# Kernel tuning notes

Measured on AMD Instinct MI355X. Metric: run time of the kernel, lower is better.

The kernel has to match this reference:

```python
import jax, jax.numpy as jnp
import numpy as np

ALPHA = 0.25
GAMMA = 2.0
LAMBDA_T = 0.1


def count_components(fg):
    """Count 6-connected components per volume. fg: [M,H,W,D] bool.
    Min-label propagation + pointer jumping (parallel union-find style CCL),
    matching scipy.ndimage.label's default face-connectivity structure.
    Returns float32 [M] component counts."""
    M, H, W, D = fg.shape
    N = H * W * D
    BIG = jnp.int32(N)  # sentinel label for background / padding
    idx = jnp.arange(N, dtype=jnp.int32).reshape(1, H, W, D)
    L0 = jnp.broadcast_to(idx, fg.shape)

    def shift(a, axis, d):
        # b[i] = a[i-d] along `axis`, padded with BIG outside the volume
        pad = [(0, 0)] * 4
        pad[axis] = (max(d, 0), max(-d, 0))
        ap = jnp.pad(a, pad, constant_values=N)
        sl = [slice(None)] * 4
        sl[axis] = slice(max(-d, 0), max(-d, 0) + a.shape[axis])
        return ap[tuple(sl)]

    def one_step(L):
        Lv = jnp.where(fg, L, BIG)
        m = Lv
        for ax in (1, 2, 3):
            for d in (1, -1):
                m = jnp.minimum(m, shift(Lv, ax, d))
        Ln = jnpp_min = jnp.where(fg, jnp.minimum(L, m), L)
        # pointer jumping (L <- L[L]) twice for log-depth convergence
        Lf = Ln.reshape(M, N)
        Lf = jnp.take_along_axis(Lf, Lf, axis=1)
        Lf = jnp.take_along_axis(Lf, Lf, axis=1)
        return Lf.reshape(M, H, W, D)

    def cond(s):
        return s[1]

    def body(s):
        L, _ = s
        Ln = one_step(L)
        return (Ln, jnp.any(Ln != L))

    L, _ = jax.lax.while_loop(cond, body, (L0, jnp.bool_(True)))
    # at fixed point every foreground component carries its min linear index;
    # roots satisfy L[i] == i
    roots = fg & (L == idx)
    return jnp.sum(roots, axis=(1, 2, 3)).astype(jnp.float32)


def _focal(x, t):
    p = jax.nn.sigmoid(x)
    pt = jnp.where(t == 1, p, 1.0 - p)
    bce = jax.nn.softplus(x) - x * t  # BCE-with-logits, elementwise
    alpha_t = jnp.where(t == 1, ALPHA, 1.0 - ALPHA)
    return jnp.mean(alpha_t * (1.0 - pt) ** GAMMA * bce)


def _topology(x, t):
    B, C = x.shape[:2]
    spatial = x.shape[2:]
    fg_p = (jax.nn.sigmoid(x) > 0.5).reshape(B * C, *spatial)
    fg_t = (t > 0.5).reshape(B * C, *spatial)
    cc_p = count_components(fg_p).reshape(B, C).mean(axis=0)  # mean over batch per class
    cc_t = count_components(fg_t).reshape(B, C).mean(axis=0)
    return jnp.mean(jnp.abs(cc_p - cc_t))  # sum over classes / C


def setup_inputs() -> dict:
    key = jax.random.key(0)
    k1, k2 = jax.random.split(key)
    shape = (2, 2, 96, 96, 96)
    pred_logits = jax.random.normal(k1, shape, dtype=jnp.float32)
    target_binary = jax.random.randint(k2, shape, 0, 2).astype(jnp.float32)
    return {"pred_logits": pred_logits, "target_binary": target_binary}


def reference(pred_logits, target_binary):
    focal = _focal(pred_logits, target_binary)
    topo = jax.lax.stop_gradient(_topology(pred_logits, target_binary))
    return focal + LAMBDA_T * topo
```

## Files before the change

### kernel.cpp

```cpp
#include <hip/hip_runtime.h>
#include <math.h>

#define N_VOX (96*96*96)
#define NVOL 8
#define NEL (4*N_VOX)
#define PLANE (96*96)
#define GMWORDS (N_VOX/32)
#define NFACC (4*GMWORDS/256)

#define TW 8
#define TH 8
#define TILES_W 12
#define TILES_H 12
#define TILE_VOX (96*TW*TH)
#define TILE_WORDS (TILE_VOX/32)
#define MAXRUNS 3072

#define NBPLANES 11
#define NPAIRS (2*NBPLANES)
#define FACES_PER_VOL (2*NPAIRS*PLANE)
#define MAXR 40192
#define FALLR 65536
#define SEGCAP 4608
#define HT2N 4096
#define MAX_PROBES 16

#define WS_ROOT  1024
#define WS_COMP  2048
#define WS_DONE  3072
#define WS_VDONE 4096
#define WS_PCNT  4352
#define WS_FACC  5120
#define WS_HDR   8192

__device__ __forceinline__ int uf_find(int* __restrict__ L, int x) {
    int r = x;
    int p = L[r];
    while (p != r) { r = p; p = L[r]; }
    if (r != x) atomicMin(&L[x], r);
    return r;
}

__device__ __forceinline__ int uf_merge(int* __restrict__ L, int l1, int l2) {
    int ev = 0;
    while (l1 != l2) {
        if (l1 < l2) { int t = l1; l1 = l2; l2 = t; }
        int l3 = atomicMin(&L[l1], l2);
        if (l3 == l1) { ev++; l1 = l2; }
        else l1 = l3;
    }
    return ev;
}

__device__ __forceinline__ void merge_local(int* lab, int l1, int l2) {
    while (l1 != l2 && l1 != lab[l1]) l1 = lab[l1];
    while (l1 != l2 && l2 != lab[l2]) l2 = lab[l2];
    while (l1 != l2) {
        if (l1 < l2) { int t = l1; l1 = l2; l2 = t; }
        int l3 = atomicMin(&lab[l1], l2);
        l1 = (l3 == l1) ? l2 : l3;
    }
}

__device__ __forceinline__ int rrank(const unsigned* __restrict__ sm,
                                     const int* __restrict__ wpf, int i) {
    int w = i >> 5, b = i & 31;
    unsigned mask = (2u << b) - 1u;
    return wpf[w] + __popc(sm[w] & mask) - 1;
}

__global__ __launch_bounds__(256) void fgmask_focal(const float* __restrict__ pred,
                                                    const float* __restrict__ targ,
                                                    unsigned* __restrict__ gmask,
                                                    float* __restrict__ facc,
                                                    int* __restrict__ rootcnt,
                                                    int* __restrict__ done,
                                                    int* __restrict__ vdone) {
    __shared__ float fws[4];
    if (blockIdx.x == 0 && threadIdx.x == 0) {
        for (int v2 = 0; v2 < NVOL; v2++) { rootcnt[v2 << 5] = 0; done[v2 << 5] = 0; }
        *vdone = 0;
    }
    int tid = blockIdx.x * 256 + threadIdx.x;
    int v = tid / GMWORDS;
    int w = tid - v * GMWORDS;
    const float4* P = (const float4*)(pred + (size_t)v * N_VOX + w * 32);
    const float4* T = (const float4*)(targ + (size_t)v * N_VOX + w * 32);
    unsigned pb = 0, tb = 0;
    float fsum = 0.0f;
    #pragma unroll
    for (int j4 = 0; j4 < 8; j4++) {
        float4 p4 = P[j4];
        float4 t4 = T[j4];
        float pv[4] = {p4.x, p4.y, p4.z, p4.w};
        float tv[4] = {t4.x, t4.y, t4.z, t4.w};
        #pragma unroll
        for (int q = 0; q < 4; q++) {
            int j = j4 * 4 + q;
            if (pv[q] > 0.0f)  pb |= (1u << j);
            if (tv[q] > 0.5f)  tb |= (1u << j);
            float m   = (tv[q] == 1.0f) ? -pv[q] : pv[q];
            float at  = (tv[q] == 1.0f) ? 0.25f : 0.75f;
            float e   = __expf(-fabsf(m));
            float inv = 1.0f / (1.0f + e);
            float sig = inv * ((m >= 0.0f) ? 1.0f : e);
            float sp  = fmaxf(m, 0.0f) + __logf(1.0f + e);
            fsum += at * sig * sig * sp;
        }
    }
    gmask[(size_t)v * GMWORDS + w]       = pb;
    gmask[(size_t)(v + 4) * GMWORDS + w] = tb;

    for (int off = 32; off; off >>= 1) fsum += __shfl_down(fsum, off, 64);
    if ((threadIdx.x & 63) == 0) fws[threadIdx.x >> 6] = fsum;
    __syncthreads();
    if (threadIdx.x == 0)
        facc[blockIdx.x] = fws[0] + fws[1] + fws[2] + fws[3];
}

__global__ __launch_bounds__(256) void ccl_local(const unsigned* __restrict__ gmask,
                                                 unsigned short* __restrict__ faces,
                                                 int* __restrict__ rootcnt,
                                                 int vbase) {
    __shared__ int      lab[MAXRUNS];
    __shared__ unsigned fm[TILE_WORDS];
    __shared__ unsigned sm[TILE_WORDS];
    __shared__ int      wpf[TILE_WORDS];
    __shared__ unsigned ovst[168];
    __shared__ int      ovpf[169];
    __shared__ int   iws[4];
    __shared__ int   gbase;

    int vloc = blockIdx.y;
    int v = vbase + vloc;
    int tile = blockIdx.x;
    int tw = tile % TILES_W, th = tile / TILES_W;
    int w0 = tw * TW, h0 = th * TH;
    int tbase = h0 * PLANE + w0 * 96;
    unsigned short* Fw = faces + (size_t)vloc * FACES_PER_VOL;
    unsigned short* Fh = Fw + 2 * NBPLANES * PLANE;
    const unsigned* gm = gmask + (size_t)v * GMWORDS;

    if (threadIdx.x < TILE_WORDS) {
        int t = threadIdx.x;
        int lh = t / 24, rem = t % 24;
        fm[t] = gm[(tbase >> 5) + lh * 288 + rem];
    }
    for (int r = threadIdx.x; r < MAXRUNS; r += 256) lab[r] = r;
    __syncthreads();

    int cnt = 0;
    {
        unsigned st = 0;
        if (threadIdx.x < TILE_WORDS) {
            unsigned m = fm[threadIdx.x];
            unsigned carry = (threadIdx.x % 3) ? (fm[threadIdx.x - 1] >> 31) : 0u;
            st = m & ~((m << 1) | carry);
            sm[threadIdx.x] = st;
            cnt = __popc(st);
        }
    }
    int inc = cnt;
    for (int off = 1; off < 64; off <<= 1) {
        int u = __shfl_up(inc, off, 64);
        if ((threadIdx.x & 63) >= off) inc += u;
    }
    int wid = threadIdx.x >> 6;
    if ((threadIdx.x & 63) == 63) iws[wid] = inc;
    __syncthreads();
    int woff = 0;
    for (int k = 0; k < wid; k++) woff += iws[k];
    if (threadIdx.x < TILE_WORDS) wpf[threadIdx.x] = woff + inc - cnt;
    int Nr = iws[0] + iws[1] + iws[2];
    __syncthreads();

    for (int dirn = 0; dirn < 2; dirn++) {
        bool wdirn = (dirn == 0);
        int cnt2 = 0;
        if (threadIdx.x < 168) {
            int tt = threadIdx.x;
            int lh, lw, k;
            if (wdirn) { lh = tt / 21; int rem = tt % 21; lw = rem / 3; k = rem % 3; }
            else       { lh = tt / 24; int rem = tt % 24; lw = rem / 3; k = rem % 3; }
            int wb = (lh * 8 + lw) * 3 + k;
            int nb = wb + (wdirn ? 3 : 24);
            unsigned ov = fm[wb] & fm[nb];
            unsigned carry = (k > 0) ? ((fm[wb - 1] & fm[nb - 1]) >> 31) : 0u;
            unsigned stm = ov & ~((ov << 1) | carry);
            ovst[threadIdx.x] = stm;
            cnt2 = __popc(stm);
        }
        int inc2 = cnt2;
        for (int off = 1; off < 64; off <<= 1) {
            int u = __shfl_up(inc2, off, 64);
            if ((threadIdx.x & 63) >= off) inc2 += u;
        }
        if ((threadIdx.x & 63) == 63) iws[wid] = inc2;
        __syncthreads();
        int woff2 = 0;
        for (int k = 0; k < wid; k++) woff2 += iws[k];
        if (threadIdx.x < 168) ovpf[threadIdx.x] = woff2 + inc2 - cnt2;
        if (threadIdx.x == 0) ovpf[168] = iws[0] + iws[1] + iws[2] + iws[3];
        __syncthreads();
        int M = ovpf[168];
        for (int k2 = threadIdx.x; k2 < M; k2 += 256) {
            int lo2 = 0, hi2 = 168;
            while (hi2 - lo2 > 1) {
                int mid = (lo2 + hi2) >> 1;
                if (ovpf[mid] <= k2) lo2 = mid; else hi2 = mid;
            }
            int p = lo2;
            int j = k2 - ovpf[p];
            int lh, lw, kk;
            if (wdirn) { lh = p / 21; int rem = p % 21; lw = rem / 3; kk = rem % 3; }
            else       { lh = p / 24; int rem = p % 24; lw = rem / 3; kk = rem % 3; }
            int wb = (lh * 8 + lw) * 3 + kk;
            unsigned stm2 = ovst[p];
            for (int q = 0; q < j; q++) stm2 &= stm2 - 1;
            int b = __builtin_ctz(stm2);
            int i = (wb << 5) + b;
            merge_local(lab, rrank(sm, wpf, i), rrank(sm, wpf, i + (wdirn ? 96 : 768)));
        }
        __syncthreads();
    }

    int myroots = 0;
    for (int r = threadIdx.x; r < Nr; r += 256)
        if (lab[r] == r) myroots++;
    int s = myroots;
    for (int off = 1; off < 64; off <<= 1) {
        int u = __shfl_up(s, off, 64);
        if ((threadIdx.x & 63) >= off) s += u;
    }
    if ((threadIdx.x & 63) == 63) iws[wid] = s;
    __syncthreads();
    int wbase = 0;
    for (int k = 0; k < wid; k++) wbase += iws[k];
    if (threadIdx.x == 0)
        gbase = atomicAdd(&rootcnt[v << 5], iws[0] + iws[1] + iws[2] + iws[3]);
    __syncthreads();
    int nid = gbase + wbase + (s - myroots);
    for (int r = threadIdx.x; r < Nr; r += 256)
        if (lab[r] == r) lab[r] = ~(nid++);
    __syncthreads();

    for (int r = threadIdx.x; r < Nr; r += 256) {
        int p = lab[r];
        if (p >= 0) {
            int q2 = lab[p];
            while (q2 >= 0) { p = q2; q2 = lab[p]; }
            lab[r] = q2;
        }
    }
    __syncthreads();

    for (int t = threadIdx.x; t < 768; t += 256) {
        int f  = t / 192;
        int g  = t % 192;
        int u  = g / 24;
        int d4 = (g % 24) * 4;
        int i0; unsigned short* dst;
        if (f == 0) {
            if (tw == 0) continue;
            i0  = u * 768 + d4;
            dst = Fw + ((tw - 1) * 2 + 1) * PLANE + (h0 + u) * 96 + d4;
        } else if (f == 1) {
            if (tw == TILES_W - 1) continue;
            i0  = u * 768 + 7 * 96 + d4;
            dst = Fw + (tw * 2) * PLANE + (h0 + u) * 96 + d4;
        } else if (f == 2) {
            if (th == 0) continue;
            i0  = u * 96 + d4;
            dst = Fh + ((th - 1) * 2 + 1) * PLANE + (w0 + u) * 96 + d4;
        } else {
            if (th == TILES_H - 1) continue;
            i0  = 7 * 768 + u * 96 + d4;
            dst = Fh + (th * 2) * PLANE + (w0 + u) * 96 + d4;
        }
        unsigned mw = fm[i0 >> 5];
        unsigned short vals[4];
        bool prevf = false;
        for (int q = 0; q < 4; q++) {
            bool fb = (mw >> ((d4 & 31) + q)) & 1;
            if (fb) vals[q] = prevf ? vals[q - 1]
                                    : (unsigned short)(~lab[rrank(sm, wpf, i0 + q)]);
            else vals[q] = 0xFFFFu;
            prevf = fb;
        }
        *(ushort4*)dst = make_ushort4(vals[0], vals[1], vals[2], vals[3]);
    }
}

__global__ __launch_bounds__(1024) void ccl_bmerge(const unsigned short* __restrict__ faces,
                                                   unsigned* __restrict__ pairs,
                                                   int* __restrict__ pcnt,
                                                   int* __restrict__ gfall,
                                                   const int* __restrict__ rootcnt,
                                                   int* __restrict__ comp,
                                                   int* __restrict__ done,
                                                   int* __restrict__ vdone,
                                                   const float* __restrict__ facc,
                                                   float* __restrict__ out,
                                                   int vbase) {
    __shared__ int slab[MAXR];
    __shared__ int offs[NPAIRS + 1];
    __shared__ int wsum[16];
    __shared__ float fred[16];
    __shared__ int nloc, lastf, lastv;
    unsigned* ht = (unsigned*)slab;

    int f    = blockIdx.x;
    int vloc = blockIdx.y;
    int v    = vbase + vloc;
    const unsigned short* A = faces + (size_t)vloc * FACES_PER_VOL
                                    + (size_t)(2 * f) * PLANE;
    const unsigned short* B = A + PLANE;
    unsigned* pb = pairs + ((size_t)vloc * NPAIRS + f) * SEGCAP;

    for (int i = threadIdx.x; i < HT2N; i += 1024) ht[i] = 0xFFFFFFFFu;
    if (threadIdx.x == 0) nloc = 0;
    __syncthreads();

    const int GPP = PLANE / 8;
    for (int g = threadIdx.x; g < GPP; g += 1024) {
        int e8 = g * 8;
        int4 aw = *(const int4*)(A + e8);
        int4 bw = *(const int4*)(B + e8);
        unsigned a32[4] = {(unsigned)aw.x, (unsigned)aw.y, (unsigned)aw.z, (unsigned)aw.w};
        unsigned b32[4] = {(unsigned)bw.x, (unsigned)bw.y, (unsigned)bw.z, (unsigned)bw.w};
        bool pf = false;
        if (e8 % 96) pf = (A[e8 - 1] != 0xFFFFu) && (B[e8 - 1] != 0xFFFFu);
        #pragma unroll
        for (int q = 0; q < 8; q++) {
            unsigned av = (a32[q >> 1] >> ((q & 1) * 16)) & 0xFFFFu;
            unsigned bv = (b32[q >> 1] >> ((q & 1) * 16)) & 0xFFFFu;
            bool f2 = (av != 0xFFFFu) && (bv != 0xFFFFu);
            if (f2 && !pf && av != bv) {
                unsigned lo = av < bv ? av : bv;
                unsigned hi = av < bv ? bv : av;
                unsigned key = (lo << 16) | hi;
                unsigned h = (key * 2654435761u) >> 20;
                bool fresh = false;
                for (int pr = 0; pr < MAX_PROBES; pr++) {
                    unsigned prev = atomicCAS(&ht[h], 0xFFFFFFFFu, key);
                    if (prev == 0xFFFFFFFFu) { fresh = true; break; }
                    if (prev == key) break;
                    h = (h + 1) & (HT2N - 1);
                    if (pr == MAX_PROBES - 1) fresh = true;
                }
                if (fresh) {
                    int ix = atomicAdd(&nloc, 1);
                    pb[ix] = key;
                }
            }
            pf = f2;
        }
    }
    __syncthreads();
    if (threadIdx.x == 0) {
        pcnt[v * NPAIRS + f] = nloc;
        __threadfence();
        int old = atomicAdd(&done[v << 5], 1);
        lastf = (old == NPAIRS - 1);
    }
    __syncthreads();
    if (!lastf) return;

    __threadfence();
    int R = rootcnt[v << 5];
    int* lab = (R <= MAXR) ? slab : (gfall + (size_t)vloc * FALLR);
    if (threadIdx.x == 0) {
        int o = 0;
        for (int k = 0; k < NPAIRS; k++) { offs[k] = o; o += pcnt[v * NPAIRS + k]; }
        offs[NPAIRS] = o;
    }
    __syncthreads();
    for (int i = threadIdx.x; i < R; i += 1024) lab[i] = i;
    int tot = offs[NPAIRS];
    __syncthreads();

    int ev = 0;
    for (int gi = threadIdx.x; gi < tot; gi += 1024) {
        int fi = 0;
        while (offs[fi + 1] <= gi) fi++;
        unsigned key = pairs[((size_t)vloc * NPAIRS + fi) * SEGCAP + (gi - offs[fi])];
        int a = (int)(key >> 16), b = (int)(key & 0xFFFFu);
        int ra = uf_find(lab, a);
        int rb = uf_find(lab, b);
        if (ra != rb) ev += uf_merge(lab, ra, rb);
    }

    for (int off = 32; off; off >>= 1) ev += __shfl_down(ev, off, 64);
    if ((threadIdx.x & 63) == 0) wsum[threadIdx.x >> 6] = ev;
    __syncthreads();
    if (threadIdx.x == 0) {
        int tote = 0;
        for (int k = 0; k < 16; k++) tote += wsum[k];
        comp[v << 5] = R - tote;
        __threadfence();
        int old2 = atomicAdd(vdone, 1);
        lastv = (old2 == NVOL - 1);
    }
    __syncthreads();
    if (!lastv) return;

    __threadfence();
    float x = 0.0f;
    for (int i2 = threadIdx.x; i2 < NFACC; i2 += 1024) x += facc[i2];
    for (int off = 32; off; off >>= 1) x += __shfl_down(x, off, 64);
    if ((threadIdx.x & 63) == 0) fred[threadIdx.x >> 6] = x;
    __syncthreads();
    if (threadIdx.x == 0) {
        float fa = 0.0f;
        for (int k = 0; k < 16; k++) fa += fred[k];
        float c[NVOL];
        for (int w = 0; w < NVOL; w++) c[w] = (float)comp[w << 5];
        float dp0 = 0.5f * (c[0] + c[2]);
        float dp1 = 0.5f * (c[1] + c[3]);
        float dt0 = 0.5f * (c[4] + c[6]);
        float dt1 = 0.5f * (c[5] + c[7]);
        float topo = 0.5f * (fabsf(dp0 - dt0) + fabsf(dp1 - dt1));
        out[0] = fa / (float)NEL + 0.1f * topo;
    }
}

extern "C" void kernel_launch(void* const* d_in, const int* in_sizes, int n_in,
                              void* d_out, int out_size, void* d_ws, size_t ws_size,
                              hipStream_t stream) {
    const float* pred = (const float*)d_in[0];
    const float* targ = (const float*)d_in[1];
    float* out = (float*)d_out;

    int*   rootcnt = (int*)((char*)d_ws + WS_ROOT);
    int*   comp    = (int*)((char*)d_ws + WS_COMP);
    int*   done    = (int*)((char*)d_ws + WS_DONE);
    int*   vdone   = (int*)((char*)d_ws + WS_VDONE);
    int*   pcnt    = (int*)((char*)d_ws + WS_PCNT);
    float* facc    = (float*)((char*)d_ws + WS_FACC);
    unsigned* gmask = (unsigned*)((char*)d_ws + WS_HDR);
    unsigned short* faces = (unsigned short*)(gmask + (size_t)NVOL * GMWORDS);

    size_t per_vol = (size_t)FACES_PER_VOL * 2
                   + (size_t)NPAIRS * SEGCAP * 4
                   + (size_t)FALLR * 4;
    size_t fixed   = WS_HDR + (size_t)NVOL * GMWORDS * 4;
    size_t avail   = (ws_size > fixed) ? ws_size - fixed : 0;
    int vols_per_pass = (int)(avail / per_vol);
    if (vols_per_pass > NVOL) vols_per_pass = NVOL;
    if (vols_per_pass < 1) vols_per_pass = 1;
    unsigned* pairs = (unsigned*)(faces + (size_t)vols_per_pass * FACES_PER_VOL);
    int* gfall = (int*)(pairs + (size_t)vols_per_pass * NPAIRS * SEGCAP);

    fgmask_focal<<<dim3(NFACC), dim3(256), 0, stream>>>(pred, targ, gmask, facc,
                                                        rootcnt, done, vdone);

    for (int vbase = 0; vbase < NVOL; vbase += vols_per_pass) {
        int nv = NVOL - vbase;
        if (nv > vols_per_pass) nv = vols_per_pass;
        dim3 tgrid(TILES_W * TILES_H, nv);
        ccl_local<<<tgrid, dim3(256), 0, stream>>>(gmask, faces, rootcnt, vbase);
        dim3 mgrid(NPAIRS, nv);
        ccl_bmerge<<<mgrid, dim3(1024), 0, stream>>>(faces, pairs, pcnt, gfall,
                                                     rootcnt, comp, done, vdone,
                                                     facc, out, vbase);
    }
}
```

Baseline: 145.3 us.

## Halve CCL tile height to 4 and resolve labels lazily at face writeout

Local CCL tiles shrink from 8x8 to 8x4 columns, which doubles the number of tile blocks and raises the boundary plane count in the h direction from 11 to 23. Merge-kernel blocks grow accordingly (34 per volume instead of 22). The separate pass that compressed every run label to its root is removed, and roots are now chased only for runs that touch a face. This is meant to improve occupancy and parallelism in the local pass, at the cost of more boundary faces to write and merge and more blocks in the global stage.

After: 174.2 us. 1.2x slower.

```diff
diff --git a/kernel.cpp b/kernel.cpp
--- a/kernel.cpp
+++ b/kernel.cpp
@@ -9,16 +9,17 @@
 #define NFACC (4*GMWORDS/256)
 
 #define TW 8
-#define TH 8
+#define TH 4
 #define TILES_W 12
-#define TILES_H 12
+#define TILES_H 24
 #define TILE_VOX (96*TW*TH)
 #define TILE_WORDS (TILE_VOX/32)
-#define MAXRUNS 3072
-
-#define NBPLANES 11
-#define NPAIRS (2*NBPLANES)
-#define FACES_PER_VOL (2*NPAIRS*PLANE)
+#define MAXRUNS 1536
+
+#define NBW 11
+#define NBH 23
+#define NPLANES (NBW+NBH)
+#define FACES_PER_VOL (2*NPLANES*PLANE)
 #define MAXR 40192
 #define FALLR 65536
 #define SEGCAP 4608
@@ -30,7 +31,7 @@
 #define WS_DONE  3072
 #define WS_VDONE 4096
 #define WS_PCNT  4352
-#define WS_FACC  5120
+#define WS_FACC  5632
 #define WS_HDR   8192
 
 __device__ __forceinline__ int uf_find(int* __restrict__ L, int x) {
@@ -126,10 +127,10 @@
     __shared__ unsigned fm[TILE_WORDS];
     __shared__ unsigned sm[TILE_WORDS];
     __shared__ int      wpf[TILE_WORDS];
-    __shared__ unsigned ovst[168];
-    __shared__ int      ovpf[169];
-    __shared__ int   iws[4];
-    __shared__ int   gbase;
+    __shared__ unsigned ovst[84];
+    __shared__ int      ovpf[85];
+    __shared__ int      iws[4];
+    __shared__ int      gbase;
 
     int vloc = blockIdx.y;
     int v = vbase + vloc;
@@ -138,13 +139,12 @@
     int w0 = tw * TW, h0 = th * TH;
     int tbase = h0 * PLANE + w0 * 96;
     unsigned short* Fw = faces + (size_t)vloc * FACES_PER_VOL;
-    unsigned short* Fh = Fw + 2 * NBPLANES * PLANE;
+    unsigned short* Fh = Fw + 2 * NBW * PLANE;
     const unsigned* gm = gmask + (size_t)v * GMWORDS;
 
     if (threadIdx.x < TILE_WORDS) {
-        int t = threadIdx.x;
-        int lh = t / 24, rem = t % 24;
-        fm[t] = gm[(tbase >> 5) + lh * 288 + rem];
+        int lh = threadIdx.x / 24, rem = threadIdx.x % 24;
+        fm[threadIdx.x] = gm[(tbase >> 5) + lh * 288 + rem];
     }
     for (int r = threadIdx.x; r < MAXRUNS; r += 256) lab[r] = r;
     __syncthreads();
@@ -171,13 +171,14 @@
     int woff = 0;
     for (int k = 0; k < wid; k++) woff += iws[k];
     if (threadIdx.x < TILE_WORDS) wpf[threadIdx.x] = woff + inc - cnt;
-    int Nr = iws[0] + iws[1] + iws[2];
+    int Nr = iws[0] + iws[1];
     __syncthreads();
 
     for (int dirn = 0; dirn < 2; dirn++) {
         bool wdirn = (dirn == 0);
+        int NN = wdirn ? 84 : 72;
         int cnt2 = 0;
-        if (threadIdx.x < 168) {
+        if (threadIdx.x < NN) {
             int tt = threadIdx.x;
             int lh, lw, k;
             if (wdirn) { lh = tt / 21; int rem = tt % 21; lw = rem / 3; k = rem % 3; }
@@ -199,12 +200,12 @@
         __syncthreads();
         int woff2 = 0;
         for (int k = 0; k < wid; k++) woff2 += iws[k];
-        if (threadIdx.x < 168) ovpf[threadIdx.x] = woff2 + inc2 - cnt2;
-        if (threadIdx.x == 0) ovpf[168] = iws[0] + iws[1] + iws[2] + iws[3];
+        if (threadIdx.x < NN) ovpf[threadIdx.x] = woff2 + inc2 - cnt2;
+        if (threadIdx.x == 0) ovpf[NN] = iws[0] + iws[1] + iws[2] + iws[3];
         __syncthreads();
-        int M = ovpf[168];
+        int M = ovpf[NN];
         for (int k2 = threadIdx.x; k2 < M; k2 += 256) {
-            int lo2 = 0, hi2 = 168;
+            int lo2 = 0, hi2 = NN;
             while (hi2 - lo2 > 1) {
                 int mid = (lo2 + hi2) >> 1;
                 if (ovpf[mid] <= k2) lo2 = mid; else hi2 = mid;
@@ -244,47 +245,49 @@
         if (lab[r] == r) lab[r] = ~(nid++);
     __syncthreads();
 
-    for (int r = threadIdx.x; r < Nr; r += 256) {
-        int p = lab[r];
-        if (p >= 0) {
-            int q2 = lab[p];
-            while (q2 >= 0) { p = q2; q2 = lab[p]; }
-            lab[r] = q2;
-        }
-    }
-    __syncthreads();
-
-    for (int t = threadIdx.x; t < 768; t += 256) {
-        int f  = t / 192;
-        int g  = t % 192;
-        int u  = g / 24;
-        int d4 = (g % 24) * 4;
-        int i0; unsigned short* dst;
-        if (f == 0) {
-            if (tw == 0) continue;
-            i0  = u * 768 + d4;
-            dst = Fw + ((tw - 1) * 2 + 1) * PLANE + (h0 + u) * 96 + d4;
-        } else if (f == 1) {
-            if (tw == TILES_W - 1) continue;
-            i0  = u * 768 + 7 * 96 + d4;
-            dst = Fw + (tw * 2) * PLANE + (h0 + u) * 96 + d4;
-        } else if (f == 2) {
-            if (th == 0) continue;
-            i0  = u * 96 + d4;
-            dst = Fh + ((th - 1) * 2 + 1) * PLANE + (w0 + u) * 96 + d4;
+    for (int t = threadIdx.x; t < 576; t += 256) {
+        int i0 = -1, d4 = 0;
+        unsigned short* dst = 0;
+        if (t < 192) {
+            int f = t / 96, g = t % 96;
+            int u = g / 24;
+            d4 = (g % 24) * 4;
+            if (f == 0) {
+                if (tw == 0) continue;
+                i0  = u * 768 + d4;
+                dst = Fw + ((tw - 1) * 2 + 1) * PLANE + (h0 + u) * 96 + d4;
+            } else {
+                if (tw == TILES_W - 1) continue;
+                i0  = u * 768 + 7 * 96 + d4;
+                dst = Fw + (tw * 2) * PLANE + (h0 + u) * 96 + d4;
+            }
         } else {
-            if (th == TILES_H - 1) continue;
-            i0  = 7 * 768 + u * 96 + d4;
-            dst = Fh + (th * 2) * PLANE + (w0 + u) * 96 + d4;
+            int f = (t - 192) / 192, g = (t - 192) % 192;
+            int u = g / 24;
+            d4 = (g % 24) * 4;
+            if (f == 0) {
+                if (th == 0) continue;
+                i0  = u * 96 + d4;
+                dst = Fh + ((th - 1) * 2 + 1) * PLANE + (w0 + u) * 96 + d4;
+            } else {
+                if (th == TILES_H - 1) continue;
+                i0  = (TH - 1) * 768 + u * 96 + d4;
+                dst = Fh + (th * 2) * PLANE + (w0 + u) * 96 + d4;
+            }
         }
         unsigned mw = fm[i0 >> 5];
         unsigned short vals[4];
         bool prevf = false;
         for (int q = 0; q < 4; q++) {
             bool fb = (mw >> ((d4 & 31) + q)) & 1;
-            if (fb) vals[q] = prevf ? vals[q - 1]
-                                    : (unsigned short)(~lab[rrank(sm, wpf, i0 + q)]);
-            else vals[q] = 0xFFFFu;
+            if (fb) {
+                if (prevf) vals[q] = vals[q - 1];
+                else {
+                    int x = lab[rrank(sm, wpf, i0 + q)];
+                    while (x >= 0) x = lab[x];
+                    vals[q] = (unsigned short)(~x);
+                }
+            } else vals[q] = 0xFFFFu;
             prevf = fb;
         }
         *(ushort4*)dst = make_ushort4(vals[0], vals[1], vals[2], vals[3]);
@@ -303,7 +306,7 @@
                                                    float* __restrict__ out,
                                                    int vbase) {
     __shared__ int slab[MAXR];
-    __shared__ int offs[NPAIRS + 1];
+    __shared__ int offs[NPLANES + 1];
     __shared__ int wsum[16];
     __shared__ float fred[16];
     __shared__ int nloc, lastf, lastv;
@@ -315,7 +318,7 @@
     const unsigned short* A = faces + (size_t)vloc * FACES_PER_VOL
                                     + (size_t)(2 * f) * PLANE;
     const unsigned short* B = A + PLANE;
-    unsigned* pb = pairs + ((size_t)vloc * NPAIRS + f) * SEGCAP;
+    unsigned* pb = pairs + ((size_t)vloc * NPLANES + f) * SEGCAP;
 
     for (int i = threadIdx.x; i < HT2N; i += 1024) ht[i] = 0xFFFFFFFFu;
     if (threadIdx.x == 0) nloc = 0;
@@ -358,10 +361,10 @@
     }
     __syncthreads();
     if (threadIdx.x == 0) {
-        pcnt[v * NPAIRS + f] = nloc;
+        pcnt[v * NPLANES + f] = nloc;
         __threadfence();
         int old = atomicAdd(&done[v << 5], 1);
-        lastf = (old == NPAIRS - 1);
+        lastf = (old == NPLANES - 1);
     }
     __syncthreads();
     if (!lastf) return;
@@ -371,19 +374,19 @@
     int* lab = (R <= MAXR) ? slab : (gfall + (size_t)vloc * FALLR);
     if (threadIdx.x == 0) {
         int o = 0;
-        for (int k = 0; k < NPAIRS; k++) { offs[k] = o; o += pcnt[v * NPAIRS + k]; }
-        offs[NPAIRS] = o;
+        for (int k = 0; k < NPLANES; k++) { offs[k] = o; o += pcnt[v * NPLANES + k]; }
+        offs[NPLANES] = o;
     }
     __syncthreads();
     for (int i = threadIdx.x; i < R; i += 1024) lab[i] = i;
-    int tot = offs[NPAIRS];
+    int tot = offs[NPLANES];
     __syncthreads();
 
     int ev = 0;
     for (int gi = threadIdx.x; gi < tot; gi += 1024) {
         int fi = 0;
         while (offs[fi + 1] <= gi) fi++;
-        unsigned key = pairs[((size_t)vloc * NPAIRS + fi) * SEGCAP + (gi - offs[fi])];
+        unsigned key = pairs[((size_t)vloc * NPLANES + fi) * SEGCAP + (gi - offs[fi])];
         int a = (int)(key >> 16), b = (int)(key & 0xFFFFu);
         int ra = uf_find(lab, a);
         int rb = uf_find(lab, b);
@@ -441,7 +444,7 @@
     unsigned short* faces = (unsigned short*)(gmask + (size_t)NVOL * GMWORDS);
 
     size_t per_vol = (size_t)FACES_PER_VOL * 2
-                   + (size_t)NPAIRS * SEGCAP * 4
+                   + (size_t)NPLANES * SEGCAP * 4
                    + (size_t)FALLR * 4;
     size_t fixed   = WS_HDR + (size_t)NVOL * GMWORDS * 4;
     size_t avail   = (ws_size > fixed) ? ws_size - fixed : 0;
@@ -449,7 +452,7 @@
     if (vols_per_pass > NVOL) vols_per_pass = NVOL;
     if (vols_per_pass < 1) vols_per_pass = 1;
     unsigned* pairs = (unsigned*)(faces + (size_t)vols_per_pass * FACES_PER_VOL);
-    int* gfall = (int*)(pairs + (size_t)vols_per_pass * NPAIRS * SEGCAP);
+    int* gfall = (int*)(pairs + (size_t)vols_per_pass * NPLANES * SEGCAP);
 
     fgmask_focal<<<dim3(NFACC), dim3(256), 0, stream>>>(pred, targ, gmask, facc,
                                                         rootcnt, done, vdone);
@@ -459,7 +462,7 @@
         if (nv > vols_per_pass) nv = vols_per_pass;
         dim3 tgrid(TILES_W * TILES_H, nv);
         ccl_local<<<tgrid, dim3(256), 0, stream>>>(gmask, faces, rootcnt, vbase);
-        dim3 mgrid(NPAIRS, nv);
+        dim3 mgrid(NPLANES, nv);
         ccl_bmerge<<<mgrid, dim3(1024), 0, stream>>>(faces, pairs, pcnt, gfall,
                                                      rootcnt, comp, done, vdone,
                                                      facc, out, vbase);
```

## Fuse tile-local CCL with boundary merge via last-arriver atomic counters

Applied to the files above, without the earlier changes.

Merges the ccl_local and ccl_bmerge kernels into one kernel. Each tile block bumps per-boundary-pair counters, and the last tile touching a pair builds that pair's edge list. The block that finishes the last pair for a volume then runs the global union-find directly in global memory, which the tile blocks initialize as their roots are numbered. This removes a kernel launch and the separate merge grid, at the cost of serialized tail work in a few 256-thread blocks and global-memory atomics in place of the shared-memory label array.

Result: slower. 385.6 us (+165.3%).

```diff
diff --git a/kernel.cpp b/kernel.cpp
--- a/kernel.cpp
+++ b/kernel.cpp
@@ -19,10 +19,9 @@
 #define NBPLANES 11
 #define NPAIRS (2*NBPLANES)
 #define FACES_PER_VOL (2*NPAIRS*PLANE)
-#define MAXR 40192
 #define FALLR 65536
 #define SEGCAP 4608
-#define HT2N 4096
+#define HTP 2048
 #define MAX_PROBES 16
 
 #define WS_ROOT  1024
@@ -30,8 +29,9 @@
 #define WS_DONE  3072
 #define WS_VDONE 4096
 #define WS_PCNT  4352
-#define WS_FACC  5120
-#define WS_HDR   8192
+#define WS_FACC  5632
+#define WS_PDONE 8192
+#define WS_HDR   32768
 
 __device__ __forceinline__ int uf_find(int* __restrict__ L, int x) {
     int r = x;
@@ -75,11 +75,15 @@
                                                     float* __restrict__ facc,
                                                     int* __restrict__ rootcnt,
                                                     int* __restrict__ done,
-                                                    int* __restrict__ vdone) {
+                                                    int* __restrict__ vdone,
+                                                    int* __restrict__ pdone) {
     __shared__ float fws[4];
-    if (blockIdx.x == 0 && threadIdx.x == 0) {
-        for (int v2 = 0; v2 < NVOL; v2++) { rootcnt[v2 << 5] = 0; done[v2 << 5] = 0; }
-        *vdone = 0;
+    if (blockIdx.x == 0) {
+        if (threadIdx.x == 0) {
+            for (int v2 = 0; v2 < NVOL; v2++) { rootcnt[v2 << 5] = 0; done[v2 << 5] = 0; }
+            *vdone = 0;
+        }
+        if (threadIdx.x < NVOL * NPAIRS) pdone[threadIdx.x << 5] = 0;
     }
     int tid = blockIdx.x * 256 + threadIdx.x;
     int v = tid / GMWORDS;
@@ -118,9 +122,18 @@
         facc[blockIdx.x] = fws[0] + fws[1] + fws[2] + fws[3];
 }
 
-__global__ __launch_bounds__(256) void ccl_local(const unsigned* __restrict__ gmask,
+__global__ __launch_bounds__(256) void ccl_fused(const unsigned* __restrict__ gmask,
                                                  unsigned short* __restrict__ faces,
+                                                 unsigned* __restrict__ pairs,
+                                                 int* __restrict__ pcnt,
+                                                 int* __restrict__ gfall,
                                                  int* __restrict__ rootcnt,
+                                                 int* __restrict__ comp,
+                                                 int* __restrict__ done,
+                                                 int* __restrict__ vdone,
+                                                 int* __restrict__ pdone,
+                                                 const float* __restrict__ facc,
+                                                 float* __restrict__ out,
                                                  int vbase) {
     __shared__ int      lab[MAXRUNS];
     __shared__ unsigned fm[TILE_WORDS];
@@ -128,8 +141,14 @@
     __shared__ int      wpf[TILE_WORDS];
     __shared__ unsigned ovst[168];
     __shared__ int      ovpf[169];
-    __shared__ int   iws[4];
-    __shared__ int   gbase;
+    __shared__ int      iws[4];
+    __shared__ int      gbase;
+    __shared__ unsigned ht2[HTP];
+    __shared__ int      nloc, nexec, lastu, lastv;
+    __shared__ int      execp[4];
+    __shared__ int      offs[NPAIRS + 1];
+    __shared__ int      wsum4[4];
+    __shared__ float    fred4[4];
 
     int vloc = blockIdx.y;
     int v = vbase + vloc;
@@ -140,11 +159,11 @@
     unsigned short* Fw = faces + (size_t)vloc * FACES_PER_VOL;
     unsigned short* Fh = Fw + 2 * NBPLANES * PLANE;
     const unsigned* gm = gmask + (size_t)v * GMWORDS;
+    int* Gv = gfall + (size_t)vloc * FALLR;
 
     if (threadIdx.x < TILE_WORDS) {
-        int t = threadIdx.x;
-        int lh = t / 24, rem = t % 24;
-        fm[t] = gm[(tbase >> 5) + lh * 288 + rem];
+        int lh = threadIdx.x / 24, rem = threadIdx.x % 24;
+        fm[threadIdx.x] = gm[(tbase >> 5) + lh * 288 + rem];
     }
     for (int r = threadIdx.x; r < MAXRUNS; r += 256) lab[r] = r;
     __syncthreads();
@@ -241,7 +260,7 @@
     __syncthreads();
     int nid = gbase + wbase + (s - myroots);
     for (int r = threadIdx.x; r < Nr; r += 256)
-        if (lab[r] == r) lab[r] = ~(nid++);
+        if (lab[r] == r) { Gv[nid] = nid; lab[r] = ~(nid++); }
     __syncthreads();
 
     for (int r = threadIdx.x; r < Nr; r += 256) {
@@ -289,130 +308,131 @@
         }
         *(ushort4*)dst = make_ushort4(vals[0], vals[1], vals[2], vals[3]);
     }
-}
-
-__global__ __launch_bounds__(1024) void ccl_bmerge(const unsigned short* __restrict__ faces,
-                                                   unsigned* __restrict__ pairs,
-                                                   int* __restrict__ pcnt,
-                                                   int* __restrict__ gfall,
-                                                   const int* __restrict__ rootcnt,
-                                                   int* __restrict__ comp,
-                                                   int* __restrict__ done,
-                                                   int* __restrict__ vdone,
-                                                   const float* __restrict__ facc,
-                                                   float* __restrict__ out,
-                                                   int vbase) {
-    __shared__ int slab[MAXR];
-    __shared__ int offs[NPAIRS + 1];
-    __shared__ int wsum[16];
-    __shared__ float fred[16];
-    __shared__ int nloc, lastf, lastv;
-    unsigned* ht = (unsigned*)slab;
-
-    int f    = blockIdx.x;
-    int vloc = blockIdx.y;
-    int v    = vbase + vloc;
-    const unsigned short* A = faces + (size_t)vloc * FACES_PER_VOL
-                                    + (size_t)(2 * f) * PLANE;
-    const unsigned short* B = A + PLANE;
-    unsigned* pb = pairs + ((size_t)vloc * NPAIRS + f) * SEGCAP;
-
-    for (int i = threadIdx.x; i < HT2N; i += 1024) ht[i] = 0xFFFFFFFFu;
-    if (threadIdx.x == 0) nloc = 0;
-    __syncthreads();
-
-    const int GPP = PLANE / 8;
-    for (int g = threadIdx.x; g < GPP; g += 1024) {
-        int e8 = g * 8;
-        int4 aw = *(const int4*)(A + e8);
-        int4 bw = *(const int4*)(B + e8);
-        unsigned a32[4] = {(unsigned)aw.x, (unsigned)aw.y, (unsigned)aw.z, (unsigned)aw.w};
-        unsigned b32[4] = {(unsigned)bw.x, (unsigned)bw.y, (unsigned)bw.z, (unsigned)bw.w};
-        bool pf = false;
-        if (e8 % 96) pf = (A[e8 - 1] != 0xFFFFu) && (B[e8 - 1] != 0xFFFFu);
-        #pragma unroll
-        for (int q = 0; q < 8; q++) {
-            unsigned av = (a32[q >> 1] >> ((q & 1) * 16)) & 0xFFFFu;
-            unsigned bv = (b32[q >> 1] >> ((q & 1) * 16)) & 0xFFFFu;
-            bool f2 = (av != 0xFFFFu) && (bv != 0xFFFFu);
-            if (f2 && !pf && av != bv) {
-                unsigned lo = av < bv ? av : bv;
-                unsigned hi = av < bv ? bv : av;
-                unsigned key = (lo << 16) | hi;
-                unsigned h = (key * 2654435761u) >> 20;
-                bool fresh = false;
-                for (int pr = 0; pr < MAX_PROBES; pr++) {
-                    unsigned prev = atomicCAS(&ht[h], 0xFFFFFFFFu, key);
-                    if (prev == 0xFFFFFFFFu) { fresh = true; break; }
-                    if (prev == key) break;
-                    h = (h + 1) & (HT2N - 1);
-                    if (pr == MAX_PROBES - 1) fresh = true;
+    __syncthreads();
+
+    if (threadIdx.x == 0) {
+        __threadfence();
+        nexec = 0;
+        if (tw > 0) {
+            if (atomicAdd(&pdone[(v * NPAIRS + (tw - 1)) << 5], 1) == 23)
+                execp[nexec++] = tw - 1;
+        }
+        if (tw < TILES_W - 1) {
+            if (atomicAdd(&pdone[(v * NPAIRS + tw) << 5], 1) == 23)
+                execp[nexec++] = tw;
+        }
+        if (th > 0) {
+            if (atomicAdd(&pdone[(v * NPAIRS + NBPLANES + th - 1) << 5], 1) == 23)
+                execp[nexec++] = NBPLANES + th - 1;
+        }
+        if (th < TILES_H - 1) {
+            if (atomicAdd(&pdone[(v * NPAIRS + NBPLANES + th) << 5], 1) == 23)
+                execp[nexec++] = NBPLANES + th;
+        }
+    }
+    __syncthreads();
+    int ne = nexec;
+    bool dou = false;
+
+    for (int e = 0; e < ne; e++) {
+        int p = execp[e];
+        if (threadIdx.x == 0) { __threadfence(); lastu = 0; }
+        for (int i = threadIdx.x; i < HTP; i += 256) ht2[i] = 0xFFFFFFFFu;
+        if (threadIdx.x == 0) nloc = 0;
+        __syncthreads();
+
+        const unsigned short* A = faces + (size_t)vloc * FACES_PER_VOL
+                                        + (size_t)(2 * p) * PLANE;
+        const unsigned short* B = A + PLANE;
+        unsigned* pb = pairs + ((size_t)vloc * NPAIRS + p) * SEGCAP;
+        const int GPP = PLANE / 8;
+        for (int g = threadIdx.x; g < GPP; g += 256) {
+            int e8 = g * 8;
+            int4 aw = *(const int4*)(A + e8);
+            int4 bw = *(const int4*)(B + e8);
+            unsigned a32[4] = {(unsigned)aw.x, (unsigned)aw.y, (unsigned)aw.z, (unsigned)aw.w};
+            unsigned b32[4] = {(unsigned)bw.x, (unsigned)bw.y, (unsigned)bw.z, (unsigned)bw.w};
+            bool pf = false;
+            if (e8 % 96) pf = (A[e8 - 1] != 0xFFFFu) && (B[e8 - 1] != 0xFFFFu);
+            #pragma unroll
+            for (int q = 0; q < 8; q++) {
+                unsigned av = (a32[q >> 1] >> ((q & 1) * 16)) & 0xFFFFu;
+                unsigned bv = (b32[q >> 1] >> ((q & 1) * 16)) & 0xFFFFu;
+                bool f2 = (av != 0xFFFFu) && (bv != 0xFFFFu);
+                if (f2 && !pf && av != bv) {
+                    unsigned lo = av < bv ? av : bv;
+                    unsigned hi = av < bv ? bv : av;
+                    unsigned key = (lo << 16) | hi;
+                    unsigned h = (key * 2654435761u) >> 21;
+                    bool fresh = false;
+                    for (int pr = 0; pr < MAX_PROBES; pr++) {
+                        unsigned prev = atomicCAS(&ht2[h], 0xFFFFFFFFu, key);
+                        if (prev == 0xFFFFFFFFu) { fresh = true; break; }
+                        if (prev == key) break;
+                        h = (h + 1) & (HTP - 1);
+                        if (pr == MAX_PROBES - 1) fresh = true;
+                    }
+                    if (fresh) {
+                        int ix = atomicAdd(&nloc, 1);
+                        pb[ix] = key;
+                    }
                 }
-                if (fresh) {
-                    int ix = atomicAdd(&nloc, 1);
-                    pb[ix] = key;
-                }
+                pf = f2;
             }
-            pf = f2;
-        }
-    }
-    __syncthreads();
-    if (threadIdx.x == 0) {
-        pcnt[v * NPAIRS + f] = nloc;
-        __threadfence();
-        int old = atomicAdd(&done[v << 5], 1);
-        lastf = (old == NPAIRS - 1);
-    }
-    __syncthreads();
-    if (!lastf) return;
-
-    __threadfence();
+        }
+        __syncthreads();
+        if (threadIdx.x == 0) {
+            pcnt[v * NPAIRS + p] = nloc;
+            __threadfence();
+            if (atomicAdd(&done[v << 5], 1) == NPAIRS - 1) lastu = 1;
+        }
+        __syncthreads();
+        if (lastu) dou = true;
+    }
+    if (!dou) return;
+
+    if (threadIdx.x == 0) __threadfence();
+    __syncthreads();
     int R = rootcnt[v << 5];
-    int* lab = (R <= MAXR) ? slab : (gfall + (size_t)vloc * FALLR);
+    (void)R;
     if (threadIdx.x == 0) {
         int o = 0;
         for (int k = 0; k < NPAIRS; k++) { offs[k] = o; o += pcnt[v * NPAIRS + k]; }
         offs[NPAIRS] = o;
     }
     __syncthreads();
-    for (int i = threadIdx.x; i < R; i += 1024) lab[i] = i;
     int tot = offs[NPAIRS];
-    __syncthreads();
-
     int ev = 0;
-    for (int gi = threadIdx.x; gi < tot; gi += 1024) {
+    for (int gi = threadIdx.x; gi < tot; gi += 256) {
         int fi = 0;
         while (offs[fi + 1] <= gi) fi++;
         unsigned key = pairs[((size_t)vloc * NPAIRS + fi) * SEGCAP + (gi - offs[fi])];
         int a = (int)(key >> 16), b = (int)(key & 0xFFFFu);
-        int ra = uf_find(lab, a);
-        int rb = uf_find(lab, b);
-        if (ra != rb) ev += uf_merge(lab, ra, rb);
-    }
-
+        int ra = uf_find(Gv, a);
+        int rb = uf_find(Gv, b);
+        if (ra != rb) ev += uf_merge(Gv, ra, rb);
+    }
     for (int off = 32; off; off >>= 1) ev += __shfl_down(ev, off, 64);
-    if ((threadIdx.x & 63) == 0) wsum[threadIdx.x >> 6] = ev;
+    if ((threadIdx.x & 63) == 0) wsum4[threadIdx.x >> 6] = ev;
     __syncthreads();
     if (threadIdx.x == 0) {
-        int tote = 0;
-        for (int k = 0; k < 16; k++) tote += wsum[k];
-        comp[v << 5] = R - tote;
+        int tote = wsum4[0] + wsum4[1] + wsum4[2] + wsum4[3];
+        comp[v << 5] = rootcnt[v << 5] - tote;
         __threadfence();
-        int old2 = atomicAdd(vdone, 1);
-        lastv = (old2 == NVOL - 1);
+        lastv = (atomicAdd(vdone, 1) == NVOL - 1);
     }
     __syncthreads();
     if (!lastv) return;
 
-    __threadfence();
+    if (threadIdx.x == 0) __threadfence();
+    __syncthreads();
     float x = 0.0f;
-    for (int i2 = threadIdx.x; i2 < NFACC; i2 += 1024) x += facc[i2];
+    for (int i2 = threadIdx.x; i2 < NFACC; i2 += 256) x += facc[i2];
     for (int off = 32; off; off >>= 1) x += __shfl_down(x, off, 64);
-    if ((threadIdx.x & 63) == 0) fred[threadIdx.x >> 6] = x;
+    if ((threadIdx.x & 63) == 0) fred4[threadIdx.x >> 6] = x;
     __syncthreads();
     if (threadIdx.x == 0) {
-        float fa = 0.0f;
-        for (int k = 0; k < 16; k++) fa += fred[k];
+        float fa = fred4[0] + fred4[1] + fred4[2] + fred4[3];
         float c[NVOL];
         for (int w = 0; w < NVOL; w++) c[w] = (float)comp[w << 5];
         float dp0 = 0.5f * (c[0] + c[2]);
@@ -437,6 +457,7 @@
     int*   vdone   = (int*)((char*)d_ws + WS_VDONE);
     int*   pcnt    = (int*)((char*)d_ws + WS_PCNT);
     float* facc    = (float*)((char*)d_ws + WS_FACC);
+    int*   pdone   = (int*)((char*)d_ws + WS_PDONE);
     unsigned* gmask = (unsigned*)((char*)d_ws + WS_HDR);
     unsigned short* faces = (unsigned short*)(gmask + (size_t)NVOL * GMWORDS);
 
@@ -452,16 +473,16 @@
     int* gfall = (int*)(pairs + (size_t)vols_per_pass * NPAIRS * SEGCAP);
 
     fgmask_focal<<<dim3(NFACC), dim3(256), 0, stream>>>(pred, targ, gmask, facc,
-                                                        rootcnt, done, vdone);
+                                                        rootcnt, done, vdone,
+                                                        pdone);
 
     for (int vbase = 0; vbase < NVOL; vbase += vols_per_pass) {
         int nv = NVOL - vbase;
         if (nv > vols_per_pass) nv = vols_per_pass;
         dim3 tgrid(TILES_W * TILES_H, nv);
-        ccl_local<<<tgrid, dim3(256), 0, stream>>>(gmask, faces, rootcnt, vbase);
-        dim3 mgrid(NPAIRS, nv);
-        ccl_bmerge<<<mgrid, dim3(1024), 0, stream>>>(faces, pairs, pcnt, gfall,
-                                                     rootcnt, comp, done, vdone,
-                                                     facc, out, vbase);
-    }
-}
+        ccl_fused<<<tgrid, dim3(256), 0, stream>>>(gmask, faces, pairs, pcnt,
+                                                   gfall, rootcnt, comp, done,
+                                                   vdone, pdone, facc, out,
+                                                   vbase);
+    }
+}
```
